# Performance work log

Measured on AMD Instinct MI355X. Metric: run time of the kernel, lower is better.

The kernel has to match this reference:

```python
import jax, jax.numpy as jnp
import numpy as np

B, S, D, H, K, L, NS, NT = 32, 512, 1024, 512, 16, 16, 16, 16
SMOOTH = 0.1
EPS = 1e-8


def setup_inputs() -> dict:
    key = jax.random.key(0)
    ks = jax.random.split(key, 16)
    hidden_layers = jax.random.normal(ks[0], (B, S, D), jnp.float32)
    span_start = jax.random.randint(ks[1], (B, K), 0, S - L).astype(jnp.int32)
    span_idx = span_start[..., None] + jnp.arange(L, dtype=jnp.int32)  # [B,K,L] in-range
    span_mask = jnp.ones((B, K, L), jnp.float32)
    span_end = span_start + (L - 1)
    length = jnp.full((B,), S, jnp.int32)
    slot_emb = jax.random.normal(ks[2], (B, K, D), jnp.float32)
    tgt_slot_embs = jax.random.normal(ks[3], (NT, D), jnp.float32)
    src_slot_ids = jax.random.randint(ks[4], (B, K), 0, NS).astype(jnp.int32)
    sc = 0.02
    p = {
        'Wih_f': jax.random.normal(ks[5], (4 * H, D)) * sc,
        'Whh_f': jax.random.normal(ks[6], (4 * H, H)) * sc,
        'bih_f': jnp.zeros((4 * H,)), 'bhh_f': jnp.zeros((4 * H,)),
        'Wih_b': jax.random.normal(ks[7], (4 * H, D)) * sc,
        'Whh_b': jax.random.normal(ks[8], (4 * H, H)) * sc,
        'bih_b': jnp.zeros((4 * H,)), 'bhh_b': jnp.zeros((4 * H,)),
        # slot_name_projection_for_slot / _for_context are eye-initialized with zero bias
        'Wps1': jnp.eye(D), 'bps1': jnp.zeros((D,)),
        'Wps2': jnp.eye(D), 'bps2': jnp.zeros((D,)),
        'Wpc1': jnp.eye(D), 'bpc1': jnp.zeros((D,)),
        'Wpc2': jnp.eye(D), 'bpc2': jnp.zeros((D,)),
    }
    inp = dict(hidden_layers=hidden_layers, span_idx=span_idx, span_mask=span_mask,
               span_start=span_start, span_end=span_end, length=length,
               slot_emb=slot_emb, tgt_slot_embs=tgt_slot_embs, src_slot_ids=src_slot_ids)
    inp.update(p)
    return inp


def _lstm_dir(x, m, Wih, Whh, bih, bhh):
    # x: [N,L,D], m: [N,L]; masked steps carry state through, emit 0
    N = x.shape[0]
    h0 = jnp.zeros((N, H), x.dtype)
    c0 = jnp.zeros((N, H), x.dtype)

    def step(carry, xm):
        h, c = carry
        xt, mt = xm
        g = xt @ Wih.T + h @ Whh.T + (bih + bhh)
        i, f, gg, o = jnp.split(g, 4, axis=-1)  # torch gate order i,f,g,o
        cn = jax.nn.sigmoid(f) * c + jax.nn.sigmoid(i) * jnp.tanh(gg)
        hn = jax.nn.sigmoid(o) * jnp.tanh(cn)
        mt = mt[:, None]
        h = mt * hn + (1.0 - mt) * h
        c = mt * cn + (1.0 - mt) * c
        return (h, c), h * mt

    _, ys = jax.lax.scan(step, (h0, c0), (jnp.swapaxes(x, 0, 1), m.T))
    return jnp.swapaxes(ys, 0, 1)  # [N,L,H]


def _mlp(x, W1, b1, W2, b2):
    # Linear -> Tanh -> (Dropout eval=identity) -> Linear
    return jnp.tanh(x @ W1.T + b1) @ W2.T + b2


def reference(hidden_layers, span_idx, span_mask, span_start, span_end, length,
              slot_emb, tgt_slot_embs, src_slot_ids,
              Wih_f, Whh_f, bih_f, bhh_f, Wih_b, Whh_b, bih_b, bhh_b,
              Wps1, bps1, Wps2, bps2, Wpc1, bpc1, Wpc2, bpc2):
    # gather span tokens: [B,K,L,D]
    spans = hidden_layers[jnp.arange(B)[:, None, None], span_idx]
    x = spans.reshape(B * K, L, D)
    m = span_mask.reshape(B * K, L)
    hf = _lstm_dir(x, m, Wih_f, Whh_f, bih_f, bhh_f)
    hb = _lstm_dir(x[:, ::-1], m[:, ::-1], Wih_b, Whh_b, bih_b, bhh_b)[:, ::-1]
    out = jnp.concatenate([hf, hb], axis=-1)           # [BK,L,2H]
    slot_feats = out.sum(axis=1).reshape(B, K, 2 * H)  # sum-pool over span

    # context attention (faithful to source: returns attn @ hidden, no softmax)
    sf = jax.lax.stop_gradient(slot_feats)
    pos = jnp.arange(S)
    cmask = (pos[None, None, :] < span_start[..., None]) | \
            ((pos[None, None, :] > span_end[..., None]) & (pos[None, None, :] < length[:, None, None]))
    attn = jnp.einsum('bkd,bsd->bks', sf, hidden_layers) * cmask.astype(hidden_layers.dtype)
    context = jnp.einsum('bks,bsd->bkd', attn, hidden_layers)  # [B,K,D]

    # smooth labels via projected slot-name embeddings (all detached in source)
    s_cat = jnp.concatenate([_mlp(slot_emb, Wps1, bps1, Wps2, bps2),
                             _mlp(slot_emb, Wpc1, bpc1, Wpc2, bpc2)], axis=-1)  # [B,K,2D]
    t_cat = jnp.concatenate([_mlp(tgt_slot_embs, Wps1, bps1, Wps2, bps2),
                             _mlp(tgt_slot_embs, Wpc1, bpc1, Wpc2, bpc2)], axis=-1)  # [NT,2D]
    s_cat = jax.lax.stop_gradient(s_cat)
    t_cat = jax.lax.stop_gradient(t_cat)
    sn = jnp.maximum(jnp.linalg.norm(s_cat, axis=-1), EPS)
    tn = jnp.maximum(jnp.linalg.norm(t_cat, axis=-1), EPS)
    sim = jnp.einsum('bkd,td->bkt', s_cat, t_cat) / (sn[..., None] * tn[None, None, :])
    sim = sim / sim.sum(axis=-1, keepdims=True) * (1.0 - SMOOTH)
    one_hot = jax.nn.one_hot(src_slot_ids, NS, dtype=sim.dtype) * SMOOTH
    labels = jnp.concatenate([one_hot, sim], axis=-1)  # [B,K,NS+NT]

    return jnp.concatenate([slot_feats, context, labels], axis=-1)  # [B,K,2H+D+NS+NT]
```

## Files before the change

kernel.cpp:

```cpp
#include <hip/hip_runtime.h>
#include <cstdio>

#define B_ 32
#define S_ 512
#define D_ 1024
#define H_ 512
#define K_ 16
#define L_ 16
#define NT_ 16
#define NSEQ 512
#define XROWS 8192
#define G4H 2048
#define OUTC 2080
#define MROWS 528

typedef unsigned short u16;
typedef __bf16 bf16x8 __attribute__((ext_vector_type(8)));
typedef float f32x4 __attribute__((ext_vector_type(4)));

__device__ inline u16 f2b(float f) {
  union { float f; unsigned u; } x; x.f = f;
  unsigned r = x.u + 0x7FFFu + ((x.u >> 16) & 1u);
  return (u16)(r >> 16);
}
__device__ inline float b2f(u16 h) {
  union { unsigned u; float f; } c; c.u = ((unsigned)h) << 16;
  return c.f;
}
__device__ inline float sigf(float x) { return 1.0f / (1.0f + expf(-x)); }
__device__ inline float wredsum(float v) {
#pragma unroll
  for (int off = 32; off > 0; off >>= 1) v += __shfl_xor(v, off);
  return v;
}
__device__ inline void gl16(const u16* g, u16* l) {
  __builtin_amdgcn_global_load_lds(
      (const __attribute__((address_space(1))) unsigned int*)g,
      (__attribute__((address_space(3))) unsigned int*)l, 16, 0, 0);
}

__global__ __launch_bounds__(256) void split_kernel(const float* __restrict__ in,
                                                    u16* __restrict__ hi,
                                                    u16* __restrict__ lo, int n) {
  int i = blockIdx.x * 256 + threadIdx.x;
  if (i >= n) return;
  float x = in[i];
  u16 h = f2b(x);
  hi[i] = h;
  lo[i] = f2b(x - b2f(h));
}

__global__ __launch_bounds__(256) void hsplit_kernel(const float* __restrict__ in,
                                                     u16* __restrict__ hi,
                                                     u16* __restrict__ lo) {
  size_t i = ((size_t)blockIdx.x * 256 + threadIdx.x) * 4;
  float4 v = *reinterpret_cast<const float4*>(in + i);
  float a[4] = {v.x, v.y, v.z, v.w};
#pragma unroll
  for (int j = 0; j < 4; ++j) {
    u16 h = f2b(a[j]);
    hi[i + j] = h;
    lo[i + j] = f2b(a[j] - b2f(h));
  }
}

__global__ __launch_bounds__(256) void icast_kernel(const float* __restrict__ W,
                                                    u16* __restrict__ out, int Kd) {
  int rp = blockIdx.x;
  int j = rp >> 2, g = rp & 3;
  const float* src = W + ((size_t)(g * H_ + j)) * Kd;
  u16* dst = out + (size_t)rp * Kd;
  for (int k = threadIdx.x; k < Kd; k += 256) dst[k] = f2b(src[k]);
}

__global__ __launch_bounds__(256) void bsum_kernel(const float* __restrict__ bih,
                                                   const float* __restrict__ bhh,
                                                   float* __restrict__ bsum) {
  int rp = blockIdx.x * 256 + threadIdx.x;
  if (rp >= G4H) return;
  int j = rp >> 2, g = rp & 3;
  bsum[rp] = bih[g * H_ + j] + bhh[g * H_ + j];
}

__global__ __launch_bounds__(256) void big_gemm_kernel(
    const u16* __restrict__ Hh, const int* __restrict__ span_idx,
    const u16* __restrict__ Wih2, u16* __restrict__ G2) {
  __shared__ u16 As[128 * 32];
  __shared__ u16 Bs[128 * 32];
  const int tid = threadIdx.x;
  const int bn = blockIdx.x * 128, bm = blockIdx.y * 128;
  const int wave = tid >> 6, lane = tid & 63;
  const int wm = (wave >> 1) * 64, wn = (wave & 1) * 64;
  const int fr = lane & 15;
  const int kg = (lane >> 4) * 8;

  const u16* asrc[2];
  const u16* bsrc[2];
  u16* adst[2];
  u16* bdst[2];
#pragma unroll
  for (int j = 0; j < 2; ++j) {
    int c = tid + 256 * j;
    int gr = bm + (c >> 2);
    int b = gr >> 8;
    int sidx = span_idx[gr];
    asrc[j] = Hh + ((size_t)(b * S_ + sidx)) * D_ + (c & 3) * 8;
    bsrc[j] = Wih2 + (size_t)(bn + (c >> 2)) * D_ + (c & 3) * 8;
    int ub = (wave * 64 + 256 * j) * 8;
    adst[j] = As + ub;
    bdst[j] = Bs + ub;
  }

  f32x4 acc[4][4] = {};
  for (int k0 = 0; k0 < D_; k0 += 32) {
    gl16(asrc[0] + k0, adst[0]);
    gl16(asrc[1] + k0, adst[1]);
    gl16(bsrc[0] + k0, bdst[0]);
    gl16(bsrc[1] + k0, bdst[1]);
    __syncthreads();
    bf16x8 af[4], bfr[4];
#pragma unroll
    for (int m = 0; m < 4; ++m)
      af[m] = *reinterpret_cast<const bf16x8*>(&As[(wm + m * 16 + fr) * 32 + kg]);
#pragma unroll
    for (int n = 0; n < 4; ++n)
      bfr[n] = *reinterpret_cast<const bf16x8*>(&Bs[(wn + n * 16 + fr) * 32 + kg]);
#pragma unroll
    for (int m = 0; m < 4; ++m)
#pragma unroll
      for (int n = 0; n < 4; ++n)
        acc[m][n] = __builtin_amdgcn_mfma_f32_16x16x32_bf16(af[m], bfr[n], acc[m][n], 0, 0, 0);
    __syncthreads();
  }
  const int ci = lane & 15;
  const int r0 = (lane >> 4) * 4;
#pragma unroll
  for (int m = 0; m < 4; ++m)
#pragma unroll
    for (int n = 0; n < 4; ++n) {
      int col = bn + wn + n * 16 + ci;
#pragma unroll
      for (int r = 0; r < 4; ++r) {
        int row = bm + wm + m * 16 + r0 + r;
        G2[(size_t)row * 4096 + col] = f2b(acc[m][n][r]);
      }
    }
}

__global__ __launch_bounds__(256) void lstm_step_kernel(
    const u16* __restrict__ hbf_in,
    const u16* __restrict__ Whhf, const u16* __restrict__ Whhb,
    const u16* __restrict__ G2,
    const float* __restrict__ bsumf, const float* __restrict__ bsumb,
    const float* __restrict__ mask,
    float* __restrict__ hst, float* __restrict__ cst,
    u16* __restrict__ hbf_out,
    float* __restrict__ sf,
    int t, int first) {
  __shared__ u16 As[64 * 32];
  __shared__ u16 Bs[64 * 32];
  const int tid = threadIdx.x;
  const int bz = blockIdx.z;
  const int treal = bz ? (L_ - 1 - t) : t;
  const u16* Whh = bz ? Whhb : Whhf;
  const float* bsum = bz ? bsumb : bsumf;
  const size_t sofs = (size_t)bz * NSEQ * H_;
  const int bm = blockIdx.y * 64, bn = blockIdx.x * 64;
  const int wave = tid >> 6, lane = tid & 63;
  const int wm = (wave >> 1) * 32, wn = (wave & 1) * 32;
  f32x4 acc[2][2] = {};
  const int fr = lane & 15;
  const int kg = (lane >> 4) * 8;

  if (!first) {
    const int c = tid;
    const u16* asrc = hbf_in + sofs + (size_t)(bm + (c >> 2)) * H_ + (c & 3) * 8;
    const u16* bsrc = Whh + (size_t)(bn + (c >> 2)) * H_ + (c & 3) * 8;
    u16* adst = As + wave * 512;
    u16* bdst = Bs + wave * 512;
    for (int k0 = 0; k0 < H_; k0 += 32) {
      gl16(asrc + k0, adst);
      gl16(bsrc + k0, bdst);
      __syncthreads();
      bf16x8 af[2], bfr[2];
#pragma unroll
      for (int m = 0; m < 2; ++m)
        af[m] = *reinterpret_cast<const bf16x8*>(&As[(wm + m * 16 + fr) * 32 + kg]);
#pragma unroll
      for (int n = 0; n < 2; ++n)
        bfr[n] = *reinterpret_cast<const bf16x8*>(&Bs[(wn + n * 16 + fr) * 32 + kg]);
#pragma unroll
      for (int m = 0; m < 2; ++m)
#pragma unroll
        for (int n = 0; n < 2; ++n)
          acc[m][n] = __builtin_amdgcn_mfma_f32_16x16x32_bf16(af[m], bfr[n], acc[m][n], 0, 0, 0);
      __syncthreads();
    }
  }

  const int ci = lane & 15;
  const int r0 = (lane >> 4) * 4;
  const int q = lane & 3;
#pragma unroll
  for (int m = 0; m < 2; ++m)
#pragma unroll
    for (int n = 0; n < 2; ++n) {
      int c = bn + wn + n * 16 + ci;
      int rowbase = bm + wm + m * 16 + r0;
      float val[4];
#pragma unroll
      for (int r = 0; r < 4; ++r) {
        int nrow = rowbase + r;
        float g2 = b2f(G2[((size_t)nrow * L_ + treal) * 4096 + (size_t)bz * 2048 + c]);
        val[r] = acc[m][n][r] + g2 + bsum[c];
      }
      float x1[4], x2[4], x3[4];
#pragma unroll
      for (int r = 0; r < 4; ++r) {
        x1[r] = __shfl_xor(val[r], 1);
        x2[r] = __shfl_xor(val[r], 2);
        x3[r] = __shfl_xor(x1[r], 2);
      }
      if (q == 0) {
        int j = c >> 2;
#pragma unroll
        for (int r = 0; r < 4; ++r) {
          int nrow = rowbase + r;
          float gi = val[r], gf = x1[r], gg = x2[r], go = x3[r];
          float mv = mask[nrow * L_ + treal];
          size_t sidx = sofs + (size_t)nrow * H_ + j;
          float co = first ? 0.f : cst[sidx];
          float ho = first ? 0.f : hst[sidx];
          float cn = sigf(gf) * co + sigf(gi) * tanhf(gg);
          float hn = sigf(go) * tanhf(cn);
          float hnew = mv * hn + (1.f - mv) * ho;
          float cnew = mv * cn + (1.f - mv) * co;
          hst[sidx] = hnew;
          cst[sidx] = cnew;
          hbf_out[sidx] = f2b(hnew);
          size_t fidx = (size_t)nrow * 1024 + bz * 512 + j;
          float contrib = hnew * mv;
          if (first) sf[fidx] = contrib;
          else sf[fidx] += contrib;
        }
      }
    }
}

__global__ __launch_bounds__(256) void copy_sf_split_kernel(const float* __restrict__ sf,
                                                            float* __restrict__ out,
                                                            u16* __restrict__ sfh,
                                                            u16* __restrict__ sfl) {
  int bk = blockIdx.x;
  for (int d = threadIdx.x; d < 1024; d += 256) {
    size_t i = (size_t)bk * 1024 + d;
    float v = sf[i];
    out[(size_t)bk * OUTC + d] = v;
    u16 h = f2b(v);
    sfh[i] = h;
    sfl[i] = f2b(v - b2f(h));
  }
}

__global__ __launch_bounds__(256) void attn_mfma_kernel(
    const u16* __restrict__ sfh, const u16* __restrict__ sfl,
    const u16* __restrict__ Hh, const u16* __restrict__ Hl,
    const int* __restrict__ sstart, const int* __restrict__ send,
    const int* __restrict__ len,
    u16* __restrict__ attn_h, u16* __restrict__ attn_l) {
  __shared__ u16 Bh[128 * 32];
  __shared__ u16 Bl[128 * 32];
  const int b = blockIdx.x;
  const int s0 = blockIdx.y * 128;
  const int tid = threadIdx.x;
  const int wave = tid >> 6, lane = tid & 63;
  const int fr = lane & 15;
  const int kg = (lane >> 4) * 8;
  f32x4 acc[2] = {};

  const u16* hsrc[2];
  const u16* lsrc[2];
  u16* hdst[2];
  u16* ldst[2];
#pragma unroll
  for (int j = 0; j < 2; ++j) {
    int c = tid + 256 * j;
    size_t goff = ((size_t)b * S_ + s0 + (c >> 2)) * D_ + (c & 3) * 8;
    hsrc[j] = Hh + goff;
    lsrc[j] = Hl + goff;
    int ub = (wave * 64 + 256 * j) * 8;
    hdst[j] = Bh + ub;
    ldst[j] = Bl + ub;
  }

  for (int k0 = 0; k0 < D_; k0 += 32) {
    gl16(hsrc[0] + k0, hdst[0]);
    gl16(hsrc[1] + k0, hdst[1]);
    gl16(lsrc[0] + k0, ldst[0]);
    gl16(lsrc[1] + k0, ldst[1]);
    __syncthreads();
    size_t aoff = ((size_t)b * 16 + fr) * D_ + k0 + kg;
    bf16x8 ah = *reinterpret_cast<const bf16x8*>(sfh + aoff);
    bf16x8 al = *reinterpret_cast<const bf16x8*>(sfl + aoff);
#pragma unroll
    for (int nt = 0; nt < 2; ++nt) {
      bf16x8 bh = *reinterpret_cast<const bf16x8*>(&Bh[(wave * 32 + nt * 16 + fr) * 32 + kg]);
      bf16x8 bl = *reinterpret_cast<const bf16x8*>(&Bl[(wave * 32 + nt * 16 + fr) * 32 + kg]);
      acc[nt] = __builtin_amdgcn_mfma_f32_16x16x32_bf16(ah, bh, acc[nt], 0, 0, 0);
      acc[nt] = __builtin_amdgcn_mfma_f32_16x16x32_bf16(ah, bl, acc[nt], 0, 0, 0);
      acc[nt] = __builtin_amdgcn_mfma_f32_16x16x32_bf16(al, bh, acc[nt], 0, 0, 0);
    }
    __syncthreads();
  }
  const int ln = len[b];
#pragma unroll
  for (int nt = 0; nt < 2; ++nt) {
    int s = s0 + wave * 32 + nt * 16 + (lane & 15);
#pragma unroll
    for (int r = 0; r < 4; ++r) {
      int krow = (lane >> 4) * 4 + r;
      int bk = b * 16 + krow;
      int st = sstart[bk], en = send[bk];
      bool cm = (s < st) || ((s > en) && (s < ln));
      float v = cm ? acc[nt][r] : 0.f;
      u16 h = f2b(v);
      size_t idx = (size_t)bk * S_ + s;
      attn_h[idx] = h;
      attn_l[idx] = f2b(v - b2f(h));
    }
  }
}

__global__ __launch_bounds__(256) void ctx_mfma_kernel(
    const u16* __restrict__ attn_h, const u16* __restrict__ attn_l,
    const u16* __restrict__ Hh, const u16* __restrict__ Hl,
    float* __restrict__ out) {
  __shared__ u16 Th[128][34];
  __shared__ u16 Tl[128][34];
  const int b = blockIdx.x;
  const int d0 = blockIdx.y * 128;
  const int tid = threadIdx.x;
  const int wave = tid >> 6, lane = tid & 63;
  const int fr = lane & 15;
  const int kg = (lane >> 4) * 8;
  f32x4 acc[2] = {};

  for (int k0 = 0; k0 < S_; k0 += 32) {
#pragma unroll
    for (int pass = 0; pass < 2; ++pass) {
      int idx = pass * 256 + tid;
      int srow = idx >> 4;
      int dch = (idx & 15) * 8;
      size_t goff = ((size_t)b * S_ + k0 + srow) * D_ + d0 + dch;
      uint4 vh = *reinterpret_cast<const uint4*>(Hh + goff);
      uint4 vl = *reinterpret_cast<const uint4*>(Hl + goff);
      const u16* ph = reinterpret_cast<const u16*>(&vh);
      const u16* pl = reinterpret_cast<const u16*>(&vl);
#pragma unroll
      for (int i = 0; i < 8; ++i) {
        Th[dch + i][srow] = ph[i];
        Tl[dch + i][srow] = pl[i];
      }
    }
    __syncthreads();
    size_t aoff = ((size_t)b * 16 + fr) * S_ + k0 + kg;
    bf16x8 ah = *reinterpret_cast<const bf16x8*>(attn_h + aoff);
    bf16x8 al = *reinterpret_cast<const bf16x8*>(attn_l + aoff);
#pragma unroll
    for (int nt = 0; nt < 2; ++nt) {
      bf16x8 bh = *reinterpret_cast<const bf16x8*>(&Th[wave * 32 + nt * 16 + fr][kg]);
      bf16x8 bl = *reinterpret_cast<const bf16x8*>(&Tl[wave * 32 + nt * 16 + fr][kg]);
      acc[nt] = __builtin_amdgcn_mfma_f32_16x16x32_bf16(ah, bh, acc[nt], 0, 0, 0);
      acc[nt] = __builtin_amdgcn_mfma_f32_16x16x32_bf16(ah, bl, acc[nt], 0, 0, 0);
      acc[nt] = __builtin_amdgcn_mfma_f32_16x16x32_bf16(al, bh, acc[nt], 0, 0, 0);
    }
    __syncthreads();
  }
#pragma unroll
  for (int nt = 0; nt < 2; ++nt) {
    int d = d0 + wave * 32 + nt * 16 + (lane & 15);
#pragma unroll
    for (int r = 0; r < 4; ++r) {
      int krow = (lane >> 4) * 4 + r;
      out[((size_t)b * 16 + krow) * OUTC + 1024 + d] = acc[nt][r];
    }
  }
}

__global__ __launch_bounds__(256) void mlp_gemm_kernel(
    const u16* __restrict__ Ah, const u16* __restrict__ Al, int a_br_stride,
    const u16* __restrict__ B0h, const u16* __restrict__ B0l,
    const u16* __restrict__ B1h, const u16* __restrict__ B1l,
    float* __restrict__ P, int M) {
  __shared__ u16 Ash[64 * 32];
  __shared__ u16 Asl[64 * 32];
  __shared__ u16 Bsh[64 * 32];
  __shared__ u16 Bsl[64 * 32];
  const int tid = threadIdx.x;
  const int zz = blockIdx.z;
  const int br = zz >> 2, ks = zz & 3;
  const u16* Ah_ = Ah + (size_t)br * a_br_stride;
  const u16* Al_ = Al + (size_t)br * a_br_stride;
  const u16* Bh = br ? B1h : B0h;
  const u16* Bl = br ? B1l : B0l;
  const int bm = blockIdx.y * 64, bn = blockIdx.x * 64;
  const int wave = tid >> 6, lane = tid & 63;
  const int wm = (wave >> 1) * 32, wn = (wave & 1) * 32;
  f32x4 acc[2][2] = {};
  const int fr = lane & 15;
  const int kg = (lane >> 4) * 8;

  const int c = tid;
  int ga = bm + (c >> 2);
  if (ga >= M) ga = M - 1;
  const u16* ahsrc = Ah_ + (size_t)ga * D_ + (c & 3) * 8;
  const u16* alsrc = Al_ + (size_t)ga * D_ + (c & 3) * 8;
  const u16* bhsrc = Bh + (size_t)(bn + (c >> 2)) * D_ + (c & 3) * 8;
  const u16* blsrc = Bl + (size_t)(bn + (c >> 2)) * D_ + (c & 3) * 8;
  u16* d0 = Ash + wave * 512;
  u16* d1 = Asl + wave * 512;
  u16* d2 = Bsh + wave * 512;
  u16* d3 = Bsl + wave * 512;

  const int kbeg = ks * 256;
  for (int k0 = kbeg; k0 < kbeg + 256; k0 += 32) {
    gl16(ahsrc + k0, d0);
    gl16(alsrc + k0, d1);
    gl16(bhsrc + k0, d2);
    gl16(blsrc + k0, d3);
    __syncthreads();
    bf16x8 afh[2], afl[2], bfh[2], bfl[2];
#pragma unroll
    for (int m = 0; m < 2; ++m) {
      afh[m] = *reinterpret_cast<const bf16x8*>(&Ash[(wm + m * 16 + fr) * 32 + kg]);
      afl[m] = *reinterpret_cast<const bf16x8*>(&Asl[(wm + m * 16 + fr) * 32 + kg]);
    }
#pragma unroll
    for (int n = 0; n < 2; ++n) {
      bfh[n] = *reinterpret_cast<const bf16x8*>(&Bsh[(wn + n * 16 + fr) * 32 + kg]);
      bfl[n] = *reinterpret_cast<const bf16x8*>(&Bsl[(wn + n * 16 + fr) * 32 + kg]);
    }
#pragma unroll
    for (int m = 0; m < 2; ++m)
#pragma unroll
      for (int n = 0; n < 2; ++n) {
        acc[m][n] = __builtin_amdgcn_mfma_f32_16x16x32_bf16(afh[m], bfh[n], acc[m][n], 0, 0, 0);
        acc[m][n] = __builtin_amdgcn_mfma_f32_16x16x32_bf16(afh[m], bfl[n], acc[m][n], 0, 0, 0);
        acc[m][n] = __builtin_amdgcn_mfma_f32_16x16x32_bf16(afl[m], bfh[n], acc[m][n], 0, 0, 0);
      }
    __syncthreads();
  }
  const int ci = lane & 15;
  const int r0 = (lane >> 4) * 4;
#pragma unroll
  for (int m = 0; m < 2; ++m)
#pragma unroll
    for (int n = 0; n < 2; ++n) {
      int col = bn + wn + n * 16 + ci;
#pragma unroll
      for (int r = 0; r < 4; ++r) {
        int row = bm + wm + m * 16 + r0 + r;
        if (row < M)
          P[((size_t)zz * MROWS + row) * D_ + col] = acc[m][n][r];
      }
    }
}

__global__ __launch_bounds__(256) void mlp_reduce_kernel(
    const float* __restrict__ P,
    const float* __restrict__ bias0, const float* __restrict__ bias1,
    u16* __restrict__ Oh, u16* __restrict__ Ol,
    float* __restrict__ Cf,
    int mode) {
  int i = blockIdx.x * 256 + threadIdx.x;
  int e = i * 4;
  const int per_br = MROWS * D_;
  int br = e / per_br;
  int rem = e - br * per_br;
  int row = rem >> 10;
  int col = rem & 1023;
  float4 s = {0.f, 0.f, 0.f, 0.f};
#pragma unroll
  for (int ks = 0; ks < 4; ++ks) {
    float4 v = *reinterpret_cast<const float4*>(
        P + ((size_t)(br * 4 + ks) * MROWS + row) * D_ + col);
    s.x += v.x; s.y += v.y; s.z += v.z; s.w += v.w;
  }
  const float* bias = br ? bias1 : bias0;
  s.x += bias[col]; s.y += bias[col + 1]; s.z += bias[col + 2]; s.w += bias[col + 3];
  if (mode == 0) {
    float a[4] = {tanhf(s.x), tanhf(s.y), tanhf(s.z), tanhf(s.w)};
    size_t o = (size_t)br * per_br + (size_t)row * D_ + col;
#pragma unroll
    for (int j = 0; j < 4; ++j) {
      u16 h = f2b(a[j]);
      Oh[o + j] = h;
      Ol[o + j] = f2b(a[j] - b2f(h));
    }
  } else {
    *reinterpret_cast<float4*>(Cf + (size_t)row * 2048 + br * 1024 + col) = s;
  }
}

__global__ __launch_bounds__(64) void labels_kernel(
    const float* __restrict__ s_cat, const float* __restrict__ t_cat,
    const int* __restrict__ src_ids, float* __restrict__ out) {
  int bk = blockIdx.x, lane = threadIdx.x;
  const float* srow = s_cat + (size_t)bk * 2048;
  float np = 0.f;
  float dots[16], tsq[16];
#pragma unroll
  for (int t = 0; t < 16; ++t) { dots[t] = 0.f; tsq[t] = 0.f; }
  for (int j = lane; j < 2048; j += 64) {
    float sv = srow[j];
    np += sv * sv;
#pragma unroll
    for (int t = 0; t < 16; ++t) {
      float tv = t_cat[t * 2048 + j];
      dots[t] += sv * tv;
      tsq[t] += tv * tv;
    }
  }
  np = wredsum(np);
#pragma unroll
  for (int t = 0; t < 16; ++t) { dots[t] = wredsum(dots[t]); tsq[t] = wredsum(tsq[t]); }
  float sn = fmaxf(sqrtf(np), 1e-8f);
  float ssum = 0.f;
  float sims[16];
#pragma unroll
  for (int t = 0; t < 16; ++t) {
    float tn = fmaxf(sqrtf(tsq[t]), 1e-8f);
    sims[t] = dots[t] / (sn * tn);
    ssum += sims[t];
  }
  float scale = 0.9f / ssum;
  if (lane < 16) {
    out[(size_t)bk * OUTC + 2064 + lane] = sims[lane] * scale;
  } else if (lane < 32) {
    int t2 = lane - 16;
    out[(size_t)bk * OUTC + 2048 + t2] = (src_ids[bk] == t2) ? 0.1f : 0.f;
  }
}

extern "C" void kernel_launch(void* const* d_in, const int* in_sizes, int n_in,
                              void* d_out, int out_size, void* d_ws, size_t ws_size,
                              hipStream_t stream) {
  const float* hidden    = (const float*)d_in[0];
  const int*   span_idx  = (const int*)d_in[1];
  const float* span_mask = (const float*)d_in[2];
  const int*   span_start= (const int*)d_in[3];
  const int*   span_end  = (const int*)d_in[4];
  const int*   length    = (const int*)d_in[5];
  const float* slot_emb  = (const float*)d_in[6];
  const float* tgt       = (const float*)d_in[7];
  const int*   src_ids   = (const int*)d_in[8];
  const float* Wih_f = (const float*)d_in[9];
  const float* Whh_f = (const float*)d_in[10];
  const float* bih_f = (const float*)d_in[11];
  const float* bhh_f = (const float*)d_in[12];
  const float* Wih_b = (const float*)d_in[13];
  const float* Whh_b = (const float*)d_in[14];
  const float* bih_b = (const float*)d_in[15];
  const float* bhh_b = (const float*)d_in[16];
  const float* Wps1 = (const float*)d_in[17];
  const float* bps1 = (const float*)d_in[18];
  const float* Wps2 = (const float*)d_in[19];
  const float* bps2 = (const float*)d_in[20];
  const float* Wpc1 = (const float*)d_in[21];
  const float* bpc1 = (const float*)d_in[22];
  const float* Wpc2 = (const float*)d_in[23];
  const float* bpc2 = (const float*)d_in[24];
  float* out = (float*)d_out;

  char* p = (char*)d_ws;
  auto alloc = [&](size_t bytes) -> void* {
    void* r = (void*)p;
    p += (bytes + 255) & ~(size_t)255;
    return r;
  };
  char*  BIG1  = (char*)alloc((size_t)XROWS * 4096 * 2);
  char*  BIG2  = (char*)alloc((size_t)2 * B_ * S_ * D_ * 2);
  float* hst   = (float*)alloc((size_t)2 * NSEQ * H_ * 4);
  float* cst   = (float*)alloc((size_t)2 * NSEQ * H_ * 4);
  u16*   hbfA  = (u16*)alloc((size_t)2 * NSEQ * H_ * 2);
  u16*   hbfB  = (u16*)alloc((size_t)2 * NSEQ * H_ * 2);
  float* sf    = (float*)alloc((size_t)NSEQ * 1024 * 4);
  u16*   sfh   = (u16*)alloc((size_t)NSEQ * 1024 * 2);
  u16*   sfl   = (u16*)alloc((size_t)NSEQ * 1024 * 2);
  u16*   attn_h= (u16*)alloc((size_t)NSEQ * S_ * 2);
  u16*   attn_l= (u16*)alloc((size_t)NSEQ * S_ * 2);
  float* CAT   = (float*)alloc((size_t)MROWS * 2048 * 4);
  u16* Wih2_i = (u16*)alloc((size_t)2 * G4H * D_ * 2);
  u16* Whhf_i = (u16*)alloc((size_t)G4H * H_ * 2);
  u16* Whhb_i = (u16*)alloc((size_t)G4H * H_ * 2);
  float* bsumf = (float*)alloc(G4H * 4);
  float* bsumb = (float*)alloc(G4H * 4);
  u16* W1sh = (u16*)alloc((size_t)D_ * D_ * 2); u16* W1sl = (u16*)alloc((size_t)D_ * D_ * 2);
  u16* W2sh = (u16*)alloc((size_t)D_ * D_ * 2); u16* W2sl = (u16*)alloc((size_t)D_ * D_ * 2);
  u16* W1ch = (u16*)alloc((size_t)D_ * D_ * 2); u16* W1cl = (u16*)alloc((size_t)D_ * D_ * 2);
  u16* W2ch = (u16*)alloc((size_t)D_ * D_ * 2); u16* W2cl = (u16*)alloc((size_t)D_ * D_ * 2);
  u16* SEh = (u16*)alloc((size_t)MROWS * D_ * 2); u16* SEl = (u16*)alloc((size_t)MROWS * D_ * 2);
  u16* T1h = (u16*)alloc((size_t)2 * MROWS * D_ * 2);
  u16* T1l = (u16*)alloc((size_t)2 * MROWS * D_ * 2);

  u16*   G2 = (u16*)BIG1;
  float* P  = (float*)BIG1;
  u16*   Hh = (u16*)BIG2;
  u16*   Hl = Hh + (size_t)B_ * S_ * D_;

  size_t need = (size_t)(p - (char*)d_ws);
  if (need > ws_size) {
    fprintf(stderr, "kernel_launch: ws too small, need %zu have %zu\n", need, ws_size);
    return;
  }

  auto split = [&](const float* src, u16* hi, u16* lo, int n) {
    split_kernel<<<(n + 255) / 256, 256, 0, stream>>>(src, hi, lo, n);
  };

  icast_kernel<<<G4H, 256, 0, stream>>>(Wih_f, Wih2_i, D_);
  icast_kernel<<<G4H, 256, 0, stream>>>(Wih_b, Wih2_i + (size_t)G4H * D_, D_);
  icast_kernel<<<G4H, 256, 0, stream>>>(Whh_f, Whhf_i, H_);
  icast_kernel<<<G4H, 256, 0, stream>>>(Whh_b, Whhb_i, H_);
  bsum_kernel<<<8, 256, 0, stream>>>(bih_f, bhh_f, bsumf);
  bsum_kernel<<<8, 256, 0, stream>>>(bih_b, bhh_b, bsumb);
  split(Wps1, W1sh, W1sl, D_ * D_);
  split(Wps2, W2sh, W2sl, D_ * D_);
  split(Wpc1, W1ch, W1cl, D_ * D_);
  split(Wpc2, W2ch, W2cl, D_ * D_);
  split(slot_emb, SEh, SEl, NSEQ * D_);
  split(tgt, SEh + (size_t)NSEQ * D_, SEl + (size_t)NSEQ * D_, NT_ * D_);

  hsplit_kernel<<<(B_ * S_ * D_) / (4 * 256), 256, 0, stream>>>(hidden, Hh, Hl);

  {
    dim3 g(4096 / 128, XROWS / 128);
    big_gemm_kernel<<<g, 256, 0, stream>>>(Hh, span_idx, Wih2_i, G2);
  }

  for (int t = 0; t < L_; ++t) {
    const u16* hin = (t & 1) ? hbfA : hbfB;
    u16* hout = (t & 1) ? hbfB : hbfA;
    dim3 g(G4H / 64, NSEQ / 64, 2);
    lstm_step_kernel<<<g, 256, 0, stream>>>(hin, Whhf_i, Whhb_i, G2, bsumf, bsumb,
                                            span_mask, hst, cst, hout, sf,
                                            t, t == 0 ? 1 : 0);
  }

  copy_sf_split_kernel<<<NSEQ, 256, 0, stream>>>(sf, out, sfh, sfl);

  {
    dim3 g(B_, S_ / 128);
    attn_mfma_kernel<<<g, 256, 0, stream>>>(sfh, sfl, Hh, Hl,
                                            span_start, span_end, length,
                                            attn_h, attn_l);
  }
  {
    dim3 g(B_, D_ / 128);
    ctx_mfma_kernel<<<g, 256, 0, stream>>>(attn_h, attn_l, Hh, Hl, out);
  }

  {
    dim3 g(D_ / 64, (MROWS + 63) / 64, 8);
    dim3 rg((2 * MROWS * D_) / (4 * 256));
    mlp_gemm_kernel<<<g, 256, 0, stream>>>(SEh, SEl, 0, W1sh, W1sl, W1ch, W1cl, P, MROWS);
    mlp_reduce_kernel<<<rg, 256, 0, stream>>>(P, bps1, bpc1, T1h, T1l, nullptr, 0);
    mlp_gemm_kernel<<<g, 256, 0, stream>>>(T1h, T1l, MROWS * D_, W2sh, W2sl, W2ch, W2cl, P, MROWS);
    mlp_reduce_kernel<<<rg, 256, 0, stream>>>(P, bps2, bpc2, nullptr, nullptr, CAT, 1);
  }

  const float* t_cat = CAT + (size_t)NSEQ * 2048;
  labels_kernel<<<NSEQ, 64, 0, stream>>>(CAT, t_cat, src_ids, out);
}
```

Before: 633.2 us.

## Batch prep kernels, fuse sf finalize into last LSTM step, use fp32 context kernel

New measurement: 639.9 us. No clear change (+1.1%).

```diff
diff --git a/kernel.cpp b/kernel.cpp
--- a/kernel.cpp
+++ b/kernel.cpp
@@ -50,6 +50,34 @@
   lo[i] = f2b(x - b2f(h));
 }
 
+__global__ __launch_bounds__(256) void sesplit_kernel(const float* __restrict__ se,
+                                                      const float* __restrict__ tg,
+                                                      u16* __restrict__ hi,
+                                                      u16* __restrict__ lo) {
+  int i = blockIdx.x * 256 + threadIdx.x;
+  float x = (i < NSEQ * D_) ? se[i] : tg[i - NSEQ * D_];
+  u16 h = f2b(x);
+  hi[i] = h;
+  lo[i] = f2b(x - b2f(h));
+}
+
+__global__ __launch_bounds__(256) void split4_kernel(
+    const float* __restrict__ s0, const float* __restrict__ s1,
+    const float* __restrict__ s2, const float* __restrict__ s3,
+    u16* __restrict__ h0, u16* __restrict__ l0,
+    u16* __restrict__ h1, u16* __restrict__ l1,
+    u16* __restrict__ h2, u16* __restrict__ l2,
+    u16* __restrict__ h3, u16* __restrict__ l3) {
+  const float* src = blockIdx.y == 0 ? s0 : blockIdx.y == 1 ? s1 : blockIdx.y == 2 ? s2 : s3;
+  u16* hi = blockIdx.y == 0 ? h0 : blockIdx.y == 1 ? h1 : blockIdx.y == 2 ? h2 : h3;
+  u16* lo = blockIdx.y == 0 ? l0 : blockIdx.y == 1 ? l1 : blockIdx.y == 2 ? l2 : l3;
+  int i = blockIdx.x * 256 + threadIdx.x;
+  float x = src[i];
+  u16 h = f2b(x);
+  hi[i] = h;
+  lo[i] = f2b(x - b2f(h));
+}
+
 __global__ __launch_bounds__(256) void hsplit_kernel(const float* __restrict__ in,
                                                      u16* __restrict__ hi,
                                                      u16* __restrict__ lo) {
@@ -64,22 +92,33 @@
   }
 }
 
-__global__ __launch_bounds__(256) void icast_kernel(const float* __restrict__ W,
-                                                    u16* __restrict__ out, int Kd) {
+__global__ __launch_bounds__(256) void wprep_kernel(
+    const float* __restrict__ Wihf, const float* __restrict__ Wihb,
+    const float* __restrict__ Whhf, const float* __restrict__ Whhb,
+    u16* __restrict__ Wih2_i, u16* __restrict__ Whhf_i, u16* __restrict__ Whhb_i) {
+  int y = blockIdx.y;
+  const float* W = y == 0 ? Wihf : y == 1 ? Wihb : y == 2 ? Whhf : Whhb;
+  int Kd = (y < 2) ? D_ : H_;
+  u16* dst = y == 0 ? Wih2_i : y == 1 ? (Wih2_i + (size_t)G4H * D_) : y == 2 ? Whhf_i : Whhb_i;
   int rp = blockIdx.x;
   int j = rp >> 2, g = rp & 3;
   const float* src = W + ((size_t)(g * H_ + j)) * Kd;
-  u16* dst = out + (size_t)rp * Kd;
-  for (int k = threadIdx.x; k < Kd; k += 256) dst[k] = f2b(src[k]);
-}
-
-__global__ __launch_bounds__(256) void bsum_kernel(const float* __restrict__ bih,
-                                                   const float* __restrict__ bhh,
-                                                   float* __restrict__ bsum) {
-  int rp = blockIdx.x * 256 + threadIdx.x;
-  if (rp >= G4H) return;
+  u16* d = dst + (size_t)rp * Kd;
+  for (int k = threadIdx.x; k < Kd; k += 256) d[k] = f2b(src[k]);
+}
+
+__global__ __launch_bounds__(256) void bsum2_kernel(
+    const float* __restrict__ bihf, const float* __restrict__ bhhf,
+    const float* __restrict__ bihb, const float* __restrict__ bhhb,
+    float* __restrict__ bsumf, float* __restrict__ bsumb) {
+  int i = blockIdx.x * 256 + threadIdx.x;
+  int dir = i >> 11;
+  int rp = i & (G4H - 1);
   int j = rp >> 2, g = rp & 3;
-  bsum[rp] = bih[g * H_ + j] + bhh[g * H_ + j];
+  const float* bi = dir ? bihb : bihf;
+  const float* bh = dir ? bhhb : bhhf;
+  float v = bi[g * H_ + j] + bh[g * H_ + j];
+  (dir ? bsumb : bsumf)[rp] = v;
 }
 
 __global__ __launch_bounds__(256) void big_gemm_kernel(
@@ -102,8 +141,10 @@
   for (int j = 0; j < 2; ++j) {
     int c = tid + 256 * j;
     int gr = bm + (c >> 2);
-    int b = gr >> 8;
-    int sidx = span_idx[gr];
+    int t = gr >> 9;
+    int seq = gr & 511;
+    int b = seq >> 4;
+    int sidx = span_idx[seq * L_ + t];
     asrc[j] = Hh + ((size_t)(b * S_ + sidx)) * D_ + (c & 3) * 8;
     bsrc[j] = Wih2 + (size_t)(bn + (c >> 2)) * D_ + (c & 3) * 8;
     int ub = (wave * 64 + 256 * j) * 8;
@@ -156,7 +197,8 @@
     float* __restrict__ hst, float* __restrict__ cst,
     u16* __restrict__ hbf_out,
     float* __restrict__ sf,
-    int t, int first) {
+    float* __restrict__ out, u16* __restrict__ sfh, u16* __restrict__ sfl,
+    int t, int first, int last) {
   __shared__ u16 As[64 * 32];
   __shared__ u16 Bs[64 * 32];
   const int tid = threadIdx.x;
@@ -211,7 +253,7 @@
 #pragma unroll
       for (int r = 0; r < 4; ++r) {
         int nrow = rowbase + r;
-        float g2 = b2f(G2[((size_t)nrow * L_ + treal) * 4096 + (size_t)bz * 2048 + c]);
+        float g2 = b2f(G2[((size_t)treal * NSEQ + nrow) * 4096 + (size_t)bz * 2048 + c]);
         val[r] = acc[m][n][r] + g2 + bsum[c];
       }
       float x1[4], x2[4], x3[4];
@@ -240,26 +282,17 @@
           hbf_out[sidx] = f2b(hnew);
           size_t fidx = (size_t)nrow * 1024 + bz * 512 + j;
           float contrib = hnew * mv;
-          if (first) sf[fidx] = contrib;
-          else sf[fidx] += contrib;
+          float snew = first ? contrib : sf[fidx] + contrib;
+          sf[fidx] = snew;
+          if (last) {
+            out[(size_t)nrow * OUTC + bz * 512 + j] = snew;
+            u16 hh = f2b(snew);
+            sfh[fidx] = hh;
+            sfl[fidx] = f2b(snew - b2f(hh));
+          }
         }
       }
     }
-}
-
-__global__ __launch_bounds__(256) void copy_sf_split_kernel(const float* __restrict__ sf,
-                                                            float* __restrict__ out,
-                                                            u16* __restrict__ sfh,
-                                                            u16* __restrict__ sfl) {
-  int bk = blockIdx.x;
-  for (int d = threadIdx.x; d < 1024; d += 256) {
-    size_t i = (size_t)bk * 1024 + d;
-    float v = sf[i];
-    out[(size_t)bk * OUTC + d] = v;
-    u16 h = f2b(v);
-    sfh[i] = h;
-    sfl[i] = f2b(v - b2f(h));
-  }
 }
 
 __global__ __launch_bounds__(256) void attn_mfma_kernel(
@@ -267,7 +300,7 @@
     const u16* __restrict__ Hh, const u16* __restrict__ Hl,
     const int* __restrict__ sstart, const int* __restrict__ send,
     const int* __restrict__ len,
-    u16* __restrict__ attn_h, u16* __restrict__ attn_l) {
+    float* __restrict__ attn_f) {
   __shared__ u16 Bh[128 * 32];
   __shared__ u16 Bl[128 * 32];
   const int b = blockIdx.x;
@@ -322,68 +355,41 @@
       int bk = b * 16 + krow;
       int st = sstart[bk], en = send[bk];
       bool cm = (s < st) || ((s > en) && (s < ln));
-      float v = cm ? acc[nt][r] : 0.f;
-      u16 h = f2b(v);
-      size_t idx = (size_t)bk * S_ + s;
-      attn_h[idx] = h;
-      attn_l[idx] = f2b(v - b2f(h));
-    }
-  }
-}
-
-__global__ __launch_bounds__(256) void ctx_mfma_kernel(
-    const u16* __restrict__ attn_h, const u16* __restrict__ attn_l,
-    const u16* __restrict__ Hh, const u16* __restrict__ Hl,
+      attn_f[(size_t)bk * S_ + s] = cm ? acc[nt][r] : 0.f;
+    }
+  }
+}
+
+__global__ __launch_bounds__(256) void ctx_f32_kernel(
+    const float* __restrict__ attn_f, const float* __restrict__ hidden,
     float* __restrict__ out) {
-  __shared__ u16 Th[128][34];
-  __shared__ u16 Tl[128][34];
+  __shared__ float att[16 * 512];
   const int b = blockIdx.x;
   const int d0 = blockIdx.y * 128;
   const int tid = threadIdx.x;
-  const int wave = tid >> 6, lane = tid & 63;
-  const int fr = lane & 15;
-  const int kg = (lane >> 4) * 8;
-  f32x4 acc[2] = {};
-
-  for (int k0 = 0; k0 < S_; k0 += 32) {
-#pragma unroll
-    for (int pass = 0; pass < 2; ++pass) {
-      int idx = pass * 256 + tid;
-      int srow = idx >> 4;
-      int dch = (idx & 15) * 8;
-      size_t goff = ((size_t)b * S_ + k0 + srow) * D_ + d0 + dch;
-      uint4 vh = *reinterpret_cast<const uint4*>(Hh + goff);
-      uint4 vl = *reinterpret_cast<const uint4*>(Hl + goff);
-      const u16* ph = reinterpret_cast<const u16*>(&vh);
-      const u16* pl = reinterpret_cast<const u16*>(&vl);
-#pragma unroll
-      for (int i = 0; i < 8; ++i) {
-        Th[dch + i][srow] = ph[i];
-        Tl[dch + i][srow] = pl[i];
-      }
-    }
-    __syncthreads();
-    size_t aoff = ((size_t)b * 16 + fr) * S_ + k0 + kg;
-    bf16x8 ah = *reinterpret_cast<const bf16x8*>(attn_h + aoff);
-    bf16x8 al = *reinterpret_cast<const bf16x8*>(attn_l + aoff);
-#pragma unroll
-    for (int nt = 0; nt < 2; ++nt) {
-      bf16x8 bh = *reinterpret_cast<const bf16x8*>(&Th[wave * 32 + nt * 16 + fr][kg]);
-      bf16x8 bl = *reinterpret_cast<const bf16x8*>(&Tl[wave * 32 + nt * 16 + fr][kg]);
-      acc[nt] = __builtin_amdgcn_mfma_f32_16x16x32_bf16(ah, bh, acc[nt], 0, 0, 0);
-      acc[nt] = __builtin_amdgcn_mfma_f32_16x16x32_bf16(ah, bl, acc[nt], 0, 0, 0);
-      acc[nt] = __builtin_amdgcn_mfma_f32_16x16x32_bf16(al, bh, acc[nt], 0, 0, 0);
-    }
-    __syncthreads();
-  }
-#pragma unroll
-  for (int nt = 0; nt < 2; ++nt) {
-    int d = d0 + wave * 32 + nt * 16 + (lane & 15);
-#pragma unroll
-    for (int r = 0; r < 4; ++r) {
-      int krow = (lane >> 4) * 4 + r;
-      out[((size_t)b * 16 + krow) * OUTC + 1024 + d] = acc[nt][r];
-    }
+  for (int i = tid; i < 16 * 512; i += 256)
+    att[i] = attn_f[((size_t)b * 16 + (i >> 9)) * S_ + (i & 511)];
+  __syncthreads();
+  const int d = d0 + (tid & 127);
+  const int sh = tid >> 7;
+  float acc[16] = {};
+  const float* hp = hidden + ((size_t)b * S_ + sh * 256) * D_ + d;
+  for (int s = 0; s < 256; ++s) {
+    float hv = hp[(size_t)s * D_];
+    int si = sh * 256 + s;
+#pragma unroll
+    for (int kr = 0; kr < 16; ++kr) acc[kr] += att[kr * 512 + si] * hv;
+  }
+  __syncthreads();
+  float* red = att;
+#pragma unroll
+  for (int kr = 0; kr < 16; ++kr) red[(sh * 16 + kr) * 128 + (tid & 127)] = acc[kr];
+  __syncthreads();
+  if (sh == 0) {
+#pragma unroll
+    for (int kr = 0; kr < 16; ++kr)
+      out[((size_t)b * 16 + kr) * OUTC + 1024 + d] =
+          red[kr * 128 + (tid & 127)] + red[(16 + kr) * 128 + (tid & 127)];
   }
 }
 
@@ -587,8 +593,7 @@
   float* sf    = (float*)alloc((size_t)NSEQ * 1024 * 4);
   u16*   sfh   = (u16*)alloc((size_t)NSEQ * 1024 * 2);
   u16*   sfl   = (u16*)alloc((size_t)NSEQ * 1024 * 2);
-  u16*   attn_h= (u16*)alloc((size_t)NSEQ * S_ * 2);
-  u16*   attn_l= (u16*)alloc((size_t)NSEQ * S_ * 2);
+  float* attn_f= (float*)alloc((size_t)NSEQ * S_ * 4);
   float* CAT   = (float*)alloc((size_t)MROWS * 2048 * 4);
   u16* Wih2_i = (u16*)alloc((size_t)2 * G4H * D_ * 2);
   u16* Whhf_i = (u16*)alloc((size_t)G4H * H_ * 2);
@@ -614,22 +619,20 @@
     return;
   }
 
-  auto split = [&](const float* src, u16* hi, u16* lo, int n) {
-    split_kernel<<<(n + 255) / 256, 256, 0, stream>>>(src, hi, lo, n);
-  };
-
-  icast_kernel<<<G4H, 256, 0, stream>>>(Wih_f, Wih2_i, D_);
-  icast_kernel<<<G4H, 256, 0, stream>>>(Wih_b, Wih2_i + (size_t)G4H * D_, D_);
-  icast_kernel<<<G4H, 256, 0, stream>>>(Whh_f, Whhf_i, H_);
-  icast_kernel<<<G4H, 256, 0, stream>>>(Whh_b, Whhb_i, H_);
-  bsum_kernel<<<8, 256, 0, stream>>>(bih_f, bhh_f, bsumf);
-  bsum_kernel<<<8, 256, 0, stream>>>(bih_b, bhh_b, bsumb);
-  split(Wps1, W1sh, W1sl, D_ * D_);
-  split(Wps2, W2sh, W2sl, D_ * D_);
-  split(Wpc1, W1ch, W1cl, D_ * D_);
-  split(Wpc2, W2ch, W2cl, D_ * D_);
-  split(slot_emb, SEh, SEl, NSEQ * D_);
-  split(tgt, SEh + (size_t)NSEQ * D_, SEl + (size_t)NSEQ * D_, NT_ * D_);
+  {
+    dim3 g(G4H, 4);
+    wprep_kernel<<<g, 256, 0, stream>>>(Wih_f, Wih_b, Whh_f, Whh_b,
+                                        Wih2_i, Whhf_i, Whhb_i);
+  }
+  bsum2_kernel<<<(2 * G4H) / 256, 256, 0, stream>>>(bih_f, bhh_f, bih_b, bhh_b,
+                                                    bsumf, bsumb);
+  {
+    dim3 g((D_ * D_) / 256, 4);
+    split4_kernel<<<g, 256, 0, stream>>>(Wps1, Wps2, Wpc1, Wpc2,
+                                         W1sh, W1sl, W2sh, W2sl,
+                                         W1ch, W1cl, W2ch, W2cl);
+  }
+  sesplit_kernel<<<(MROWS * D_) / 256, 256, 0, stream>>>(slot_emb, tgt, SEh, SEl);
 
   hsplit_kernel<<<(B_ * S_ * D_) / (4 * 256), 256, 0, stream>>>(hidden, Hh, Hl);
 
@@ -644,20 +647,18 @@
     dim3 g(G4H / 64, NSEQ / 64, 2);
     lstm_step_kernel<<<g, 256, 0, stream>>>(hin, Whhf_i, Whhb_i, G2, bsumf, bsumb,
                                             span_mask, hst, cst, hout, sf,
-                                            t, t == 0 ? 1 : 0);
-  }
-
-  copy_sf_split_kernel<<<NSEQ, 256, 0, stream>>>(sf, out, sfh, sfl);
+                                            out, sfh, sfl,
+                                            t, t == 0 ? 1 : 0, t == L_ - 1 ? 1 : 0);
+  }
 
   {
     dim3 g(B_, S_ / 128);
     attn_mfma_kernel<<<g, 256, 0, stream>>>(sfh, sfl, Hh, Hl,
-                                            span_start, span_end, length,
-                                            attn_h, attn_l);
+                                            span_start, span_end, length, attn_f);
   }
   {
     dim3 g(B_, D_ / 128);
-    ctx_mfma_kernel<<<g, 256, 0, stream>>>(attn_h, attn_l, Hh, Hl, out);
+    ctx_f32_kernel<<<g, 256, 0, stream>>>(attn_f, hidden, out);
   }
 
   {
```
